# Performance work log

Hardware: AMD Instinct MI355X
Metric: run time of the kernel (lower is better)

The kernel has to match this reference:

```python
import jax, jax.numpy as jnp
import numpy as np

# ---- static configuration (mirrors EarthSpecificBlock/EarthAttention3D) ----
WS = (2, 6, 12)                 # window_size (Z, H, W)
DIM = 192
HEADS = 6
DEPTH = 2
B, Z, H, W = 1, 8, 91, 180      # token grid entering the layer
PAD_H = (WS[1] - H % WS[1]) % WS[1]   # 5
PAD_W = (WS[2] - W % WS[2]) % WS[2]   # 0
HP, WP = H + PAD_H, W + PAD_W         # 96, 180
TOK = WS[0] * WS[1] * WS[2]           # 144 tokens per window
NZ, NH, NW = Z // WS[0], HP // WS[1], WP // WS[2]   # 4, 16, 15
TYPE_W = NZ * NH                      # 64 window types (Z x lat)
BIAS_ROWS = (2 * WS[2] - 1) * WS[1] * WS[1] * WS[0] * WS[0]  # 3312


def _construct_index():
    """Position index into the earth-specific bias table (EarthAttention3D._construct_index)."""
    zi = np.arange(WS[0]); zj = -np.arange(WS[0]) * WS[0]
    hi = np.arange(WS[1]); hj = -np.arange(WS[1]) * WS[1]
    w = np.arange(WS[2])
    c1 = np.stack(np.meshgrid(zi, hi, w, indexing='ij')).reshape(3, -1)
    c2 = np.stack(np.meshgrid(zj, hj, w, indexing='ij')).reshape(3, -1)
    coords = (c1[:, :, None] - c2[:, None, :]).transpose(1, 2, 0)
    coords[:, :, 2] += WS[2] - 1
    coords[:, :, 1] *= 2 * WS[2] - 1
    coords[:, :, 0] *= (2 * WS[2] - 1) * WS[1] * WS[1]
    return coords.sum(-1).reshape(-1)   # (TOK*TOK,)


def _gen_mask():
    """Shifted-window attention mask (gen_mask), shape (1, NW, TYPE_W, 1, TOK, TOK)."""
    m = np.zeros((1, Z, HP, WP, 1), np.float32)
    zs = (slice(0, -WS[0]), slice(-WS[0], -WS[0] // 2), slice(-WS[0] // 2, None))
    hs = (slice(0, -WS[1]), slice(-WS[1], -WS[1] // 2), slice(-WS[1] // 2, None))
    cnt = 0
    for zsl in zs:
        for hsl in hs:
            m[:, zsl, hsl, :, :] = cnt
            cnt += 1
    mw = m.reshape(1, NZ, WS[0], NH, WS[1], NW, WS[2], 1).transpose(0, 1, 3, 5, 2, 4, 6, 7)
    mw = mw.reshape(1, NZ, NH, NW, TOK)
    am = mw[:, :, :, :, None, :] - mw[:, :, :, :, :, None]
    am = np.where(am != 0, np.float32(-100.0), np.float32(0.0))
    return am.transpose(0, 3, 1, 2, 4, 5).reshape(1, NW, TYPE_W, 1, TOK, TOK)


POS_IDX = jnp.asarray(_construct_index())
MASK = jnp.asarray(_gen_mask())


def _ln(x, g, b):
    m = x.mean(-1, keepdims=True)
    v = ((x - m) ** 2).mean(-1, keepdims=True)
    return (x - m) * jax.lax.rsqrt(v + 1e-5) * g + b


def _block(x, qkv_w, qkv_b, proj_w, proj_b, bias_tab, g1, b1, g2, b2, w1, bm1, w2, bm2, roll):
    shortcut = x
    x = jnp.pad(x, ((0, 0), (0, 0), (0, PAD_H), (0, PAD_W), (0, 0)))
    if roll:
        x = jnp.roll(x, (-(WS[0] // 2), -(WS[1] // 2), -(WS[2] // 2)), axis=(1, 2, 3))
    # window partition: (B, NW, TYPE_W, TOK, C)
    xw = x.reshape(B, NZ, WS[0], NH, WS[1], NW, WS[2], DIM).transpose(0, 5, 1, 3, 2, 4, 6, 7)
    xw = xw.reshape(B, NW, TYPE_W, TOK, DIM)
    dh = DIM // HEADS
    qkv = (xw @ qkv_w + qkv_b).reshape(B, NW, TYPE_W, TOK, 3, HEADS, dh)
    qkv = qkv.transpose(4, 0, 1, 2, 5, 3, 6)   # (3, B, NW, TYPE_W, HEADS, TOK, dh)
    q, k, v = qkv[0], qkv[1], qkv[2]
    q = q * (dh ** -0.5)
    attn = jnp.einsum('bwphid,bwphjd->bwphij', q, k)
    bias = bias_tab[POS_IDX].reshape(TOK, TOK, TYPE_W, HEADS).transpose(2, 3, 0, 1)
    attn = attn + bias
    if roll:
        attn = attn + MASK
    attn = jax.nn.softmax(attn, axis=-1)
    out = jnp.einsum('bwphij,bwphjd->bwphid', attn, v)
    out = out.transpose(0, 1, 2, 4, 3, 5).reshape(B, NW, TYPE_W, TOK, DIM)
    out = out @ proj_w + proj_b
    # window merge back to (B, Z, HP, WP, C)
    x = out.reshape(B, NW, NZ, NH, WS[0], WS[1], WS[2], DIM).transpose(0, 2, 4, 3, 5, 1, 6, 7)
    x = x.reshape(B, Z, HP, WP, DIM)
    if roll:
        x = jnp.roll(x, (WS[0] // 2, WS[1] // 2, WS[2] // 2), axis=(1, 2, 3))
    x = x[:, :, :H, :W]
    x = shortcut + _ln(x, g1, b1)           # post-norm residual, as in source
    h = jax.nn.gelu(x @ w1 + bm1, approximate=False)
    h = h @ w2 + bm2
    return x + _ln(h, g2, b2)


def setup_inputs() -> dict:
    key = jax.random.key(0)
    ks = jax.random.split(key, 8)
    s = 0.02
    return {
        'x': jax.random.normal(ks[0], (B, Z, H, W, DIM), jnp.float32),
        'qkv_w': jax.random.normal(ks[1], (DEPTH, DIM, 3 * DIM), jnp.float32) * s,
        'qkv_b': jnp.zeros((DEPTH, 3 * DIM), jnp.float32),
        'proj_w': jax.random.normal(ks[2], (DEPTH, DIM, DIM), jnp.float32) * s,
        'proj_b': jnp.zeros((DEPTH, DIM), jnp.float32),
        'bias_tab': jax.random.normal(ks[3], (DEPTH, BIAS_ROWS, TYPE_W, HEADS), jnp.float32) * s,
        'norm1_g': jnp.ones((DEPTH, DIM), jnp.float32),
        'norm1_b': jnp.zeros((DEPTH, DIM), jnp.float32),
        'norm2_g': jnp.ones((DEPTH, DIM), jnp.float32),
        'norm2_b': jnp.zeros((DEPTH, DIM), jnp.float32),
        'mlp_w1': jax.random.normal(ks[4], (DEPTH, DIM, 4 * DIM), jnp.float32) * s,
        'mlp_b1': jnp.zeros((DEPTH, 4 * DIM), jnp.float32),
        'mlp_w2': jax.random.normal(ks[5], (DEPTH, 4 * DIM, DIM), jnp.float32) * s,
        'mlp_b2': jnp.zeros((DEPTH, DIM), jnp.float32),
    }


def reference(x, qkv_w, qkv_b, proj_w, proj_b, bias_tab, norm1_g, norm1_b,
              norm2_g, norm2_b, mlp_w1, mlp_b1, mlp_w2, mlp_b2):
    for i in range(DEPTH):
        x = _block(x, qkv_w[i], qkv_b[i], proj_w[i], proj_b[i], bias_tab[i],
                   norm1_g[i], norm1_b[i], norm2_g[i], norm2_b[i],
                   mlp_w1[i], mlp_b1[i], mlp_w2[i], mlp_b2[i], roll=(i % 2 == 1))
    return x
```

## Files before the change

### kernel.cpp

```cpp
#include <hip/hip_runtime.h>
#include <math.h>

#define NTOK   131040
#define NTOKW  138240

typedef __attribute__((ext_vector_type(8))) short bf16x8;
typedef __attribute__((ext_vector_type(8))) unsigned short u16x8;
typedef __attribute__((ext_vector_type(4))) float f32x4;
typedef __attribute__((ext_vector_type(2))) float f32x2;

__device__ __forceinline__ float b2f(unsigned short u){
  union { unsigned u; float f; } v; v.u = ((unsigned)u) << 16; return v.f;
}
__device__ __forceinline__ unsigned short f2b(float f){
  union { float f; unsigned u; } v; v.f = f;
  unsigned r = v.u + 0x7FFFu + ((v.u >> 16) & 1u);
  return (unsigned short)(r >> 16);
}
__device__ __forceinline__ float gelu_fast(float x){
  float t = 0.79788456080286536f * (x + 0.044715f * x * x * x);
  float e = __expf(2.0f * t);
  float th = 1.0f - 2.0f * __builtin_amdgcn_rcpf(e + 1.0f);
  return 0.5f * x * (1.0f + th);
}
__device__ __forceinline__ unsigned pk_bf16(float lo, float hi){
  unsigned r;
  asm("v_cvt_pk_bf16_f32 %0, %1, %2" : "=v"(r) : "v"(lo), "v"(hi));
  return r;
}
__device__ __forceinline__ void lds_barrier(){
  asm volatile("s_waitcnt lgkmcnt(0)" ::: "memory");
  __builtin_amdgcn_sched_barrier(0);
  __builtin_amdgcn_s_barrier();
  __builtin_amdgcn_sched_barrier(0);
}

__global__ __launch_bounds__(256) void transp(const float* __restrict__ src,
                                              unsigned short* __restrict__ dst,
                                              int K, int N){
  int i = blockIdx.x*256 + threadIdx.x;
  if (i < K*N){
    int n = i / K, k = i % K;
    dst[i] = f2b(src[(size_t)k*N + n]);
  }
}

__global__ __launch_bounds__(256) void bias_pre(
    const float* __restrict__ btab,
    unsigned short* __restrict__ bw,
    int roll)
{
  int gid = blockIdx.x*256 + threadIdx.x;
  int e    = gid % 40;
  int rem  = gid / 40;
  int lane = rem % 64;
  int rem2 = rem / 64;
  int wv   = rem2 % 9;
  int slice= rem2 / 9;
  unsigned short out = 0;
  if (e < 36){
    int ct = e >> 2, r = e & 3;
    int i = wv*16 + (lane>>4)*4 + r;
    int j = ct*16 + (lane & 15);
    int tw = slice / 6, head = slice % 6;
    int ia = i/72, ib = (i%72)/12, ic = i%12;
    int ja = j/72, jb = (j%72)/12, jc = j%12;
    int idx = (ia + 2*ja)*828 + (ib + 6*jb)*23 + (ic - jc + 11);
    float v = btab[(size_t)idx*384 + tw*6 + head];
    if (roll){
      int nz = tw >> 4, nh = tw & 15;
      int zi = nz*2+ia, hi = nh*6+ib, zj = nz*2+ja, hj = nh*6+jb;
      int ri = 3*((zi<6)?0:((zi<7)?1:2)) + ((hi<90)?0:((hi<93)?1:2));
      int rj = 3*((zj<6)?0:((zj<7)?1:2)) + ((hj<90)?0:((hj<93)?1:2));
      if (ri != rj) v -= 100.0f;
    }
    out = f2b(v);
  }
  int vec = e >> 3, elem = e & 7;
  size_t di = ((((size_t)slice*9 + wv)*5 + vec)*64 + lane)*8 + elem;
  bw[di] = out;
}

__global__ __launch_bounds__(256) void gather_win(const float* __restrict__ x,
                                                  unsigned short* __restrict__ xw,
                                                  int roll){
  int gid = blockIdx.x*256 + threadIdx.x;
  int row = gid / 24;
  int dp  = gid % 24;
  int tok = row % 144;
  int wt  = row / 144;
  int tw  = wt & 63;
  int w   = wt >> 6;
  int nz = tw >> 4, nh = tw & 15;
  int wz = tok / 72; int rem = tok % 72; int wh = rem / 12; int ww = rem % 12;
  int z = nz*2 + wz, h = nh*6 + wh, wc = w*12 + ww;
  if (roll){ z = (z+1)&7; h = (h+3)%96; wc = (wc+6)%180; }
  int d0 = dp*8;
  u16x8 o;
  if (h < 91){
    const float* s = x + ((size_t)((z*91 + h)*180 + wc))*192 + d0;
    #pragma unroll
    for (int i=0;i<8;i++) o[i] = f2b(s[i]);
  } else {
    #pragma unroll
    for (int i=0;i<8;i++) o[i] = 0;
  }
  *(u16x8*)(xw + (size_t)row*192 + d0) = o;
}

__global__ __launch_bounds__(512) void gemm_k192(
    const unsigned short* __restrict__ A,
    const unsigned short* __restrict__ Bt,
    const float* __restrict__ bias,
    unsigned short* __restrict__ C,
    int N)
{
  __shared__ unsigned short Bst[192][200];
  int m0 = blockIdx.x * 128;
  int n0 = blockIdx.y * 192;
  int t = threadIdx.x;
  int lane = t & 63, w = t >> 6;
  int wm = w >> 2, wn = w & 3;
  int lg = lane >> 4, lr = lane & 15;

  #pragma unroll
  for (int i=0;i<9;i++){
    int idx = t + i*512;
    int r = idx / 24, c = (idx % 24)*8;
    *(u16x8*)&Bst[r][c] = *(const u16x8*)(Bt + (size_t)(n0 + r)*192 + c);
  }
  __syncthreads();

  const unsigned short* aRow = A + (size_t)(m0 + wm*64 + lr)*192 + lg*8;

  f32x4 acc[4][3];
  #pragma unroll
  for (int a=0;a<4;a++)
    #pragma unroll
    for (int b=0;b<3;b++) acc[a][b] = (f32x4){0.f,0.f,0.f,0.f};

  bf16x8 aP[2][6];
  #pragma unroll
  for (int ks=0; ks<6; ks++) aP[0][ks] = *(const bf16x8*)(aRow + ks*32);

  #pragma unroll
  for (int rt=0; rt<4; rt++){
    if (rt < 3){
      const unsigned short* an = aRow + (size_t)(rt+1)*16*192;
      #pragma unroll
      for (int ks=0; ks<6; ks++) aP[(rt+1)&1][ks] = *(const bf16x8*)(an + ks*32);
    }
    #pragma unroll
    for (int ks=0; ks<6; ks++){
      bf16x8 b0 = *(const bf16x8*)&Bst[wn*48 +      lr][ks*32 + lg*8];
      bf16x8 b1 = *(const bf16x8*)&Bst[wn*48 + 16 + lr][ks*32 + lg*8];
      bf16x8 b2 = *(const bf16x8*)&Bst[wn*48 + 32 + lr][ks*32 + lg*8];
      bf16x8 af = aP[rt&1][ks];
      acc[rt][0] = __builtin_amdgcn_mfma_f32_16x16x32_bf16(af, b0, acc[rt][0], 0,0,0);
      acc[rt][1] = __builtin_amdgcn_mfma_f32_16x16x32_bf16(af, b1, acc[rt][1], 0,0,0);
      acc[rt][2] = __builtin_amdgcn_mfma_f32_16x16x32_bf16(af, b2, acc[rt][2], 0,0,0);
    }
  }

  #pragma unroll
  for (int rt=0; rt<4; rt++){
    #pragma unroll
    for (int fn=0; fn<3; fn++){
      int colg = n0 + wn*48 + fn*16 + lr;
      float bv = bias[colg];
      #pragma unroll
      for (int r=0;r<4;r++){
        int rowg = m0 + wm*64 + rt*16 + lg*4 + r;
        C[(size_t)rowg*N + colg] = f2b(acc[rt][fn][r] + bv);
      }
    }
  }
}

__global__ __launch_bounds__(576) void attn_win(
    const unsigned short* __restrict__ qkv,
    const unsigned short* __restrict__ bw,
    unsigned short* __restrict__ outp)
{
  __shared__ union {
    struct { unsigned short Qs[144][32]; unsigned short Ks[144][40]; } qk;
    unsigned short Ps[144][160];
  } U;
  __shared__ unsigned short Vst[32][160];

  int b = blockIdx.x;
  int head = b % 6;
  int wt = b / 6;
  int tw = wt & 63;
  int t = threadIdx.x;
  int lane = t & 63;
  int wv = t >> 6;
  int lg = lane >> 4, lr = lane & 15;

  {
    int tok = t >> 2, c0 = (t & 3)*8;
    size_t base = ((size_t)wt*144 + tok)*576 + head*32 + c0;
    u16x8 qv = *(const u16x8*)(qkv + base);
    u16x8 kv = *(const u16x8*)(qkv + base + 192);
    u16x8 vv = *(const u16x8*)(qkv + base + 384);
    u16x8 qs;
    #pragma unroll
    for (int i=0;i<8;i++) qs[i] = f2b(b2f(qv[i]) * 0.17677669529663687f);
    *(u16x8*)&U.qk.Qs[tok][c0] = qs;
    *(u16x8*)&U.qk.Ks[tok][c0] = kv;
    #pragma unroll
    for (int i=0;i<8;i++) Vst[c0+i][tok] = vv[i];
  }
  if (t < 512) Vst[t >> 4][144 + (t & 15)] = 0;

  u16x8 bv0, bv1, bv2, bv3, bv4;
  {
    size_t sbase = ((((size_t)(tw*6 + head))*9 + wv)*5*64 + lane)*8;
    bv0 = *(const u16x8*)(bw + sbase);
    bv1 = *(const u16x8*)(bw + sbase + 64*8);
    bv2 = *(const u16x8*)(bw + sbase + 2*64*8);
    bv3 = *(const u16x8*)(bw + sbase + 3*64*8);
    bv4 = *(const u16x8*)(bw + sbase + 4*64*8);
  }
  __syncthreads();

  float s[9][4];
  {
    bf16x8 a = *(const bf16x8*)&U.qk.Qs[wv*16 + lr][lg*8];
    #pragma unroll
    for (int ct=0; ct<9; ct++){
      bf16x8 bb = *(const bf16x8*)&U.qk.Ks[ct*16 + lr][lg*8];
      f32x4 d = {0.f,0.f,0.f,0.f};
      d = __builtin_amdgcn_mfma_f32_16x16x32_bf16(a, bb, d, 0,0,0);
      s[ct][0]=d[0]; s[ct][1]=d[1]; s[ct][2]=d[2]; s[ct][3]=d[3];
    }
  }

  #pragma unroll
  for (int ct=0; ct<9; ct++){
    #pragma unroll
    for (int r=0;r<4;r++){
      const int e = ct*4 + r;
      unsigned short bu =
        (e < 8)  ? bv0[e & 7] :
        (e < 16) ? bv1[e & 7] :
        (e < 24) ? bv2[e & 7] :
        (e < 32) ? bv3[e & 7] : bv4[e & 7];
      s[ct][r] += b2f(bu);
    }
  }

  float mx[4] = {-1e30f,-1e30f,-1e30f,-1e30f};
  #pragma unroll
  for (int ct=0; ct<9; ct++)
    #pragma unroll
    for (int r=0;r<4;r++) mx[r] = fmaxf(mx[r], s[ct][r]);
  #pragma unroll
  for (int off=1; off<16; off<<=1)
    #pragma unroll
    for (int r=0;r<4;r++) mx[r] = fmaxf(mx[r], __shfl_xor(mx[r], off));
  float sm[4] = {0.f,0.f,0.f,0.f};
  #pragma unroll
  for (int ct=0; ct<9; ct++)
    #pragma unroll
    for (int r=0;r<4;r++){ s[ct][r] = __expf(s[ct][r] - mx[r]); sm[r] += s[ct][r]; }
  #pragma unroll
  for (int off=1; off<16; off<<=1)
    #pragma unroll
    for (int r=0;r<4;r++) sm[r] += __shfl_xor(sm[r], off);
  float inv[4];
  #pragma unroll
  for (int r=0;r<4;r++) inv[r] = 1.0f / sm[r];

  lds_barrier();

  #pragma unroll
  for (int ct=0; ct<9; ct++)
    #pragma unroll
    for (int r=0;r<4;r++)
      U.Ps[wv*16 + lg*4 + r][ct*16 + lr] = f2b(s[ct][r] * inv[r]);
  #pragma unroll
  for (int r=0;r<4;r++) U.Ps[wv*16 + lg*4 + r][144 + lr] = 0;
  __syncthreads();

  #pragma unroll
  for (int ct2=0; ct2<2; ct2++){
    f32x4 o = {0.f,0.f,0.f,0.f};
    #pragma unroll
    for (int kt=0; kt<5; kt++){
      bf16x8 a  = *(const bf16x8*)&U.Ps[wv*16 + lr][kt*32 + lg*8];
      bf16x8 bb = *(const bf16x8*)&Vst[ct2*16 + lr][kt*32 + lg*8];
      o = __builtin_amdgcn_mfma_f32_16x16x32_bf16(a, bb, o, 0,0,0);
    }
    size_t rb = ((size_t)wt*144 + wv*16 + lg*4)*192 + head*32 + ct2*16 + lr;
    #pragma unroll
    for (int r=0;r<4;r++) outp[rb + (size_t)r*192] = f2b(o[r]);
  }
}

__global__ __launch_bounds__(256) void unwin_ln(
  const unsigned short* __restrict__ ywin,
  const float* __restrict__ xsrc,
  const float* __restrict__ g, const float* __restrict__ bb,
  float* __restrict__ outf, unsigned short* __restrict__ outb, int roll)
{
  int tok = blockIdx.x*4 + (threadIdx.x>>6);
  if (tok >= NTOK) return;
  int lane = threadIdx.x & 63;
  int z = tok / (91*180);
  int rem = tok % (91*180);
  int h = rem / 180, wc = rem % 180;
  int zz=z, hh=h, ww=wc;
  if (roll){ zz = (z+7)&7; hh = (h+93)%96; ww = (wc+174)%180; }
  int nz = zz>>1, wz = zz&1;
  int nh = hh/6,  wh = hh%6;
  int nw = ww/12, w2 = ww%12;
  size_t row = ((size_t)(nw*64 + nz*16 + nh))*144 + wz*72 + wh*12 + w2;
  const unsigned short* yr = ywin + row*192;
  float v[3]; float s=0.f, ss=0.f;
  #pragma unroll
  for (int i=0;i<3;i++){ v[i] = b2f(yr[lane + i*64]); s += v[i]; ss += v[i]*v[i]; }
  #pragma unroll
  for (int off=32; off>=1; off>>=1){ s += __shfl_xor(s, off); ss += __shfl_xor(ss, off); }
  float mean = s * (1.0f/192.0f);
  float var = ss * (1.0f/192.0f) - mean*mean;
  float rinv = rsqrtf(var + 1e-5f);
  size_t tb = (size_t)tok*192;
  #pragma unroll
  for (int i=0;i<3;i++){
    int d = lane + i*64;
    float o = xsrc[tb + d] + ((v[i]-mean)*rinv*g[d] + bb[d]);
    outf[tb+d] = o;
    outb[tb+d] = f2b(o);
  }
}

__global__ __launch_bounds__(256) void mlp_fused_ln(
    const unsigned short* __restrict__ A,
    const unsigned short* __restrict__ W1t,
    const float* __restrict__ bias1,
    const unsigned short* __restrict__ W2t,
    const float* __restrict__ mbias2,
    const float* __restrict__ xmid,
    const float* __restrict__ lng,
    const float* __restrict__ lnb,
    float* __restrict__ outF,
    int M)
{
  __shared__ unsigned short W1s[32][204];
  __shared__ unsigned short W2s[192][44];
  __shared__ unsigned short Hs[4][32][40];
  __shared__ float b1s[768];
  __shared__ float eps[576];
  int m0 = blockIdx.x*128;
  int t = threadIdx.x, lane = t & 63, w = t >> 6;
  int lg = lane >> 4, lr = lane & 15;

  bf16x8 afrA[6], afrB[6];
  {
    int ra = m0 + w*32 + lr, rb = ra + 16;
    if (ra < M){
      const unsigned short* ap = A + (size_t)ra*192 + lg*8;
      #pragma unroll
      for (int ks=0; ks<6; ks++) afrA[ks] = *(const bf16x8*)(ap + ks*32);
    } else {
      #pragma unroll
      for (int ks=0; ks<6; ks++)
        #pragma unroll
        for (int j=0;j<8;j++) afrA[ks][j] = 0;
    }
    if (rb < M){
      const unsigned short* ap = A + (size_t)rb*192 + lg*8;
      #pragma unroll
      for (int ks=0; ks<6; ks++) afrB[ks] = *(const bf16x8*)(ap + ks*32);
    } else {
      #pragma unroll
      for (int ks=0; ks<6; ks++)
        #pragma unroll
        for (int j=0;j<8;j++) afrB[ks][j] = 0;
    }
  }

  b1s[t] = bias1[t];
  b1s[t + 256] = bias1[t + 256];
  b1s[t + 512] = bias1[t + 512];
  if (t < 192){ eps[t] = mbias2[t]; eps[192 + t] = lng[t]; eps[384 + t] = lnb[t]; }

  int i1r[3], i1c[3], i2r[3], i2c[3];
  #pragma unroll
  for (int i=0;i<3;i++){
    int idx = t + i*256;
    i1r[i] = idx/24; i1c[i] = (idx%24)*8;
    i2r[i] = idx/4;  i2c[i] = (idx&3)*8;
  }

  u16x8 w1r[3], w2r[3];
  #pragma unroll
  for (int i=0;i<3;i++){
    w1r[i] = *(const u16x8*)(W1t + (size_t)i1r[i]*192 + i1c[i]);
    w2r[i] = *(const u16x8*)(W2t + (size_t)i2r[i]*768 + i2c[i]);
  }

  f32x4 accA[12], accB[12];
  #pragma unroll
  for (int i=0;i<12;i++){ accA[i] = (f32x4){0.f,0.f,0.f,0.f}; accB[i] = (f32x4){0.f,0.f,0.f,0.f}; }

  for (int it=0; it<24; ++it){
    int hc = it*32;
    #pragma unroll
    for (int i=0;i<3;i++){
      *(u16x8*)&W1s[i1r[i]][i1c[i]] = w1r[i];
      *(u16x8*)&W2s[i2r[i]][i2c[i]] = w2r[i];
    }
    if (it < 23){
      int hc2 = hc + 32;
      #pragma unroll
      for (int i=0;i<3;i++){
        w1r[i] = *(const u16x8*)(W1t + (size_t)(hc2 + i1r[i])*192 + i1c[i]);
        w2r[i] = *(const u16x8*)(W2t + (size_t)i2r[i]*768 + hc2 + i2c[i]);
      }
    }
    lds_barrier();

    f32x4 h0a = (f32x4){0.f,0.f,0.f,0.f}, h1a = h0a, h0b = h0a, h1b = h0a;
    #pragma unroll
    for (int ks=0; ks<6; ks++){
      bf16x8 b0  = *(const bf16x8*)&W1s[2*lr    ][ks*32 + lg*8];
      bf16x8 b1f = *(const bf16x8*)&W1s[2*lr + 1][ks*32 + lg*8];
      h0a = __builtin_amdgcn_mfma_f32_16x16x32_bf16(afrA[ks], b0,  h0a, 0,0,0);
      h1a = __builtin_amdgcn_mfma_f32_16x16x32_bf16(afrA[ks], b1f, h1a, 0,0,0);
      h0b = __builtin_amdgcn_mfma_f32_16x16x32_bf16(afrB[ks], b0,  h0b, 0,0,0);
      h1b = __builtin_amdgcn_mfma_f32_16x16x32_bf16(afrB[ks], b1f, h1b, 0,0,0);
    }
    float bb0 = b1s[hc + 2*lr];
    float bb1 = b1s[hc + 2*lr + 1];
    #pragma unroll
    for (int r=0;r<4;r++){
      *(unsigned*)&Hs[w][lg*4 + r][2*lr] =
          pk_bf16(gelu_fast(h0a[r] + bb0), gelu_fast(h1a[r] + bb1));
      *(unsigned*)&Hs[w][16 + lg*4 + r][2*lr] =
          pk_bf16(gelu_fast(h0b[r] + bb0), gelu_fast(h1b[r] + bb1));
    }
    bf16x8 paA = *(const bf16x8*)&Hs[w][lr][lg*8];
    bf16x8 paB = *(const bf16x8*)&Hs[w][16 + lr][lg*8];
    #pragma unroll
    for (int f=0; f<6; f++){
      bf16x8 c0 = *(const bf16x8*)&W2s[f*32 + 2*lr    ][lg*8];
      bf16x8 c1 = *(const bf16x8*)&W2s[f*32 + 2*lr + 1][lg*8];
      accA[2*f]   = __builtin_amdgcn_mfma_f32_16x16x32_bf16(paA, c0, accA[2*f],   0,0,0);
      accA[2*f+1] = __builtin_amdgcn_mfma_f32_16x16x32_bf16(paA, c1, accA[2*f+1], 0,0,0);
      accB[2*f]   = __builtin_amdgcn_mfma_f32_16x16x32_bf16(paB, c0, accB[2*f],   0,0,0);
      accB[2*f+1] = __builtin_amdgcn_mfma_f32_16x16x32_bf16(paB, c1, accB[2*f+1], 0,0,0);
    }
    lds_barrier();
  }

  #pragma unroll
  for (int gsel=0; gsel<2; gsel++){
    f32x4* acc = gsel ? accB : accA;
    #pragma unroll
    for (int r=0;r<4;r++){
      int row = m0 + w*32 + gsel*16 + lg*4 + r;
      float s = 0.f, ss = 0.f;
      #pragma unroll
      for (int f=0; f<6; f++){
        float v0 = acc[2*f][r]   + eps[f*32 + 2*lr];
        float v1 = acc[2*f+1][r] + eps[f*32 + 2*lr + 1];
        s += v0 + v1; ss += v0*v0 + v1*v1;
      }
      #pragma unroll
      for (int off=1; off<16; off<<=1){ s += __shfl_xor(s, off); ss += __shfl_xor(ss, off); }
      float mean = s * (1.0f/192.0f);
      float var  = ss * (1.0f/192.0f) - mean*mean;
      float rinv = rsqrtf(var + 1e-5f);
      if (row < M){
        size_t base = (size_t)row*192;
        #pragma unroll
        for (int f=0; f<6; f++){
          int c0 = f*32 + 2*lr;
          float v0 = acc[2*f][r]   + eps[c0];
          float v1 = acc[2*f+1][r] + eps[c0 + 1];
          f32x2 xm = *(const f32x2*)&xmid[base + c0];
          f32x2 o;
          o[0] = xm[0] + (v0 - mean)*rinv*eps[192 + c0]     + eps[384 + c0];
          o[1] = xm[1] + (v1 - mean)*rinv*eps[192 + c0 + 1] + eps[384 + c0 + 1];
          *(f32x2*)&outF[base + c0] = o;
        }
      }
    }
  }
}

extern "C" void kernel_launch(void* const* d_in, const int* in_sizes, int n_in,
                              void* d_out, int out_size, void* d_ws, size_t ws_size,
                              hipStream_t stream)
{
  const float* x_in    = (const float*)d_in[0];
  const float* qkvw    = (const float*)d_in[1];
  const float* qkvbias = (const float*)d_in[2];
  const float* projw   = (const float*)d_in[3];
  const float* projbias= (const float*)d_in[4];
  const float* btab    = (const float*)d_in[5];
  const float* n1g = (const float*)d_in[6];
  const float* n1b = (const float*)d_in[7];
  const float* n2g = (const float*)d_in[8];
  const float* n2b = (const float*)d_in[9];
  const float* w1  = (const float*)d_in[10];
  const float* b1  = (const float*)d_in[11];
  const float* w2  = (const float*)d_in[12];
  const float* b2  = (const float*)d_in[13];
  float* outp = (float*)d_out;

  const size_t REG_A = (size_t)NTOKW*192;
  const size_t REG_B = (size_t)NTOKW*576;
  const size_t W_QT  = (size_t)2*576*192;
  const size_t W_PT  = (size_t)2*192*192;
  const size_t W_1T  = (size_t)2*768*192;
  const size_t W_2T  = (size_t)2*192*768;
  const size_t TOT_SH = REG_A + REG_B + W_QT + W_PT + W_1T + W_2T;
  const size_t NEEDED = TOT_SH*2 + (size_t)NTOK*192*4;
  if (ws_size < NEEDED) return;

  unsigned short* ws16 = (unsigned short*)d_ws;
  size_t off = 0;
  unsigned short* regA = ws16 + off; off += REG_A;
  unsigned short* regB = ws16 + off; off += REG_B;
  unsigned short* wqt  = ws16 + off; off += W_QT;
  unsigned short* wpt  = ws16 + off; off += W_PT;
  unsigned short* w1t  = ws16 + off; off += W_1T;
  unsigned short* w2t  = ws16 + off; off += W_2T;
  float* xmidf = (float*)(ws16 + off);
  unsigned short* bw = (unsigned short*)xmidf;

  for (int dep=0; dep<2; dep++){
    transp<<<(192*576+255)/256,256,0,stream>>>(qkvw + (size_t)dep*192*576,
                                               wqt + (size_t)dep*576*192, 192, 576);
    transp<<<(192*192+255)/256,256,0,stream>>>(projw + (size_t)dep*192*192,
                                               wpt + (size_t)dep*192*192, 192, 192);
    transp<<<(192*768+255)/256,256,0,stream>>>(w1 + (size_t)dep*192*768,
                                               w1t + (size_t)dep*768*192, 192, 768);
    transp<<<(768*192+255)/256,256,0,stream>>>(w2 + (size_t)dep*768*192,
                                               w2t + (size_t)dep*192*768, 768, 192);
  }

  for (int dep=0; dep<2; dep++){
    int roll = dep;
    const float* xs = (dep==0) ? x_in : outp;
    float* xout = outp;

    gather_win<<<NTOKW*24/256, 256, 0, stream>>>(xs, regA, roll);

    dim3 g1(NTOKW/128, 3);
    gemm_k192<<<g1, 512, 0, stream>>>(regA, wqt + (size_t)dep*576*192,
                                      qkvbias + dep*576, regB, 576);

    bias_pre<<<(384*9*64*40)/256, 256, 0, stream>>>(btab + (size_t)dep*3312*384, bw, roll);

    attn_win<<<960*6, 576, 0, stream>>>(regB, bw, regA);

    dim3 g2(NTOKW/128, 1);
    gemm_k192<<<g2, 512, 0, stream>>>(regA, wpt + (size_t)dep*192*192,
                                      projbias + dep*192, regB, 192);

    unwin_ln<<<NTOK/4, 256, 0, stream>>>(regB, xs, n1g + dep*192, n1b + dep*192,
                                         xmidf, regA, roll);

    mlp_fused_ln<<<(NTOK+127)/128, 256, 0, stream>>>(
        regA, w1t + (size_t)dep*768*192, b1 + dep*768,
        w2t + (size_t)dep*192*768, b2 + dep*192,
        xmidf, n2g + dep*192, n2b + dep*192, xout, NTOK);
  }
}
```

Before: 1.185 ms.

## Double-buffer MLP weight tiles and software-pipeline first GEMM ahead of second

```diff
diff --git a/kernel.cpp b/kernel.cpp
--- a/kernel.cpp
+++ b/kernel.cpp
@@ -335,7 +335,7 @@
   }
 }
 
-__global__ __launch_bounds__(256) void mlp_fused_ln(
+__global__ __launch_bounds__(512) void mlp_fused_ln(
     const unsigned short* __restrict__ A,
     const unsigned short* __restrict__ W1t,
     const float* __restrict__ bias1,
@@ -347,12 +347,12 @@
     float* __restrict__ outF,
     int M)
 {
-  __shared__ unsigned short W1s[32][204];
-  __shared__ unsigned short W2s[192][44];
-  __shared__ unsigned short Hs[4][32][40];
+  __shared__ unsigned short W1s[2][32][196];
+  __shared__ unsigned short W2s[2][192][44];
+  __shared__ unsigned short Hs[8][32][40];
   __shared__ float b1s[768];
   __shared__ float eps[576];
-  int m0 = blockIdx.x*128;
+  int m0 = blockIdx.x*256;
   int t = threadIdx.x, lane = t & 63, w = t >> 6;
   int lg = lane >> 4, lr = lane & 15;
 
@@ -382,56 +382,75 @@
   }
 
   b1s[t] = bias1[t];
-  b1s[t + 256] = bias1[t + 256];
-  b1s[t + 512] = bias1[t + 512];
+  if (t < 256) b1s[512 + t] = bias1[512 + t];
   if (t < 192){ eps[t] = mbias2[t]; eps[192 + t] = lng[t]; eps[384 + t] = lnb[t]; }
 
-  int i1r[3], i1c[3], i2r[3], i2c[3];
-  #pragma unroll
-  for (int i=0;i<3;i++){
-    int idx = t + i*256;
+  int i1r[2], i1c[2], i2r[2], i2c[2];
+  #pragma unroll
+  for (int i=0;i<2;i++){
+    int idx = t + i*512;
     i1r[i] = idx/24; i1c[i] = (idx%24)*8;
     i2r[i] = idx/4;  i2c[i] = (idx&3)*8;
   }
-
-  u16x8 w1r[3], w2r[3];
-  #pragma unroll
-  for (int i=0;i<3;i++){
-    w1r[i] = *(const u16x8*)(W1t + (size_t)i1r[i]*192 + i1c[i]);
-    w2r[i] = *(const u16x8*)(W2t + (size_t)i2r[i]*768 + i2c[i]);
-  }
+  bool g2nd = (t + 512) < 768;
+
+  {
+    *(u16x8*)&W1s[0][i1r[0]][i1c[0]] = *(const u16x8*)(W1t + (size_t)i1r[0]*192 + i1c[0]);
+    *(u16x8*)&W1s[1][i1r[0]][i1c[0]] = *(const u16x8*)(W1t + (size_t)(32 + i1r[0])*192 + i1c[0]);
+    *(u16x8*)&W2s[0][i2r[0]][i2c[0]] = *(const u16x8*)(W2t + (size_t)i2r[0]*768 + i2c[0]);
+    if (g2nd){
+      *(u16x8*)&W1s[0][i1r[1]][i1c[1]] = *(const u16x8*)(W1t + (size_t)i1r[1]*192 + i1c[1]);
+      *(u16x8*)&W1s[1][i1r[1]][i1c[1]] = *(const u16x8*)(W1t + (size_t)(32 + i1r[1])*192 + i1c[1]);
+      *(u16x8*)&W2s[0][i2r[1]][i2c[1]] = *(const u16x8*)(W2t + (size_t)i2r[1]*768 + i2c[1]);
+    }
+  }
+  lds_barrier();
+
+  u16x8 w1r[2], w2r[2];
+  w1r[0] = *(const u16x8*)(W1t + (size_t)(64 + i1r[0])*192 + i1c[0]);
+  w2r[0] = *(const u16x8*)(W2t + (size_t)i2r[0]*768 + 32 + i2c[0]);
+  if (g2nd){
+    w1r[1] = *(const u16x8*)(W1t + (size_t)(64 + i1r[1])*192 + i1c[1]);
+    w2r[1] = *(const u16x8*)(W2t + (size_t)i2r[1]*768 + 32 + i2c[1]);
+  }
+
+  f32x4 h0a = (f32x4){0.f,0.f,0.f,0.f}, h1a = h0a, h0b = h0a, h1b = h0a;
+  #pragma unroll
+  for (int ks=0; ks<6; ks++){
+    bf16x8 b0  = *(const bf16x8*)&W1s[0][2*lr    ][ks*32 + lg*8];
+    bf16x8 b1f = *(const bf16x8*)&W1s[0][2*lr + 1][ks*32 + lg*8];
+    h0a = __builtin_amdgcn_mfma_f32_16x16x32_bf16(afrA[ks], b0,  h0a, 0,0,0);
+    h1a = __builtin_amdgcn_mfma_f32_16x16x32_bf16(afrA[ks], b1f, h1a, 0,0,0);
+    h0b = __builtin_amdgcn_mfma_f32_16x16x32_bf16(afrB[ks], b0,  h0b, 0,0,0);
+    h1b = __builtin_amdgcn_mfma_f32_16x16x32_bf16(afrB[ks], b1f, h1b, 0,0,0);
+  }
+  lds_barrier();
 
   f32x4 accA[12], accB[12];
   #pragma unroll
   for (int i=0;i<12;i++){ accA[i] = (f32x4){0.f,0.f,0.f,0.f}; accB[i] = (f32x4){0.f,0.f,0.f,0.f}; }
 
   for (int it=0; it<24; ++it){
+    int cur = it & 1, nxt = cur ^ 1;
+
+    if (it < 22){
+      *(u16x8*)&W1s[cur][i1r[0]][i1c[0]] = w1r[0];
+      if (g2nd) *(u16x8*)&W1s[cur][i1r[1]][i1c[1]] = w1r[1];
+    }
+    if (it < 23){
+      *(u16x8*)&W2s[nxt][i2r[0]][i2c[0]] = w2r[0];
+      if (g2nd) *(u16x8*)&W2s[nxt][i2r[1]][i2c[1]] = w2r[1];
+    }
+    if (it < 21){
+      w1r[0] = *(const u16x8*)(W1t + (size_t)((it+3)*32 + i1r[0])*192 + i1c[0]);
+      if (g2nd) w1r[1] = *(const u16x8*)(W1t + (size_t)((it+3)*32 + i1r[1])*192 + i1c[1]);
+    }
+    if (it < 22){
+      w2r[0] = *(const u16x8*)(W2t + (size_t)i2r[0]*768 + (it+2)*32 + i2c[0]);
+      if (g2nd) w2r[1] = *(const u16x8*)(W2t + (size_t)i2r[1]*768 + (it+2)*32 + i2c[1]);
+    }
+
     int hc = it*32;
-    #pragma unroll
-    for (int i=0;i<3;i++){
-      *(u16x8*)&W1s[i1r[i]][i1c[i]] = w1r[i];
-      *(u16x8*)&W2s[i2r[i]][i2c[i]] = w2r[i];
-    }
-    if (it < 23){
-      int hc2 = hc + 32;
-      #pragma unroll
-      for (int i=0;i<3;i++){
-        w1r[i] = *(const u16x8*)(W1t + (size_t)(hc2 + i1r[i])*192 + i1c[i]);
-        w2r[i] = *(const u16x8*)(W2t + (size_t)i2r[i]*768 + hc2 + i2c[i]);
-      }
-    }
-    lds_barrier();
-
-    f32x4 h0a = (f32x4){0.f,0.f,0.f,0.f}, h1a = h0a, h0b = h0a, h1b = h0a;
-    #pragma unroll
-    for (int ks=0; ks<6; ks++){
-      bf16x8 b0  = *(const bf16x8*)&W1s[2*lr    ][ks*32 + lg*8];
-      bf16x8 b1f = *(const bf16x8*)&W1s[2*lr + 1][ks*32 + lg*8];
-      h0a = __builtin_amdgcn_mfma_f32_16x16x32_bf16(afrA[ks], b0,  h0a, 0,0,0);
-      h1a = __builtin_amdgcn_mfma_f32_16x16x32_bf16(afrA[ks], b1f, h1a, 0,0,0);
-      h0b = __builtin_amdgcn_mfma_f32_16x16x32_bf16(afrB[ks], b0,  h0b, 0,0,0);
-      h1b = __builtin_amdgcn_mfma_f32_16x16x32_bf16(afrB[ks], b1f, h1b, 0,0,0);
-    }
     float bb0 = b1s[hc + 2*lr];
     float bb1 = b1s[hc + 2*lr + 1];
     #pragma unroll
@@ -443,15 +462,31 @@
     }
     bf16x8 paA = *(const bf16x8*)&Hs[w][lr][lg*8];
     bf16x8 paB = *(const bf16x8*)&Hs[w][16 + lr][lg*8];
+
+    f32x4 hn0a = (f32x4){0.f,0.f,0.f,0.f}, hn1a = hn0a, hn0b = hn0a, hn1b = hn0a;
+    if (it < 23){
+      #pragma unroll
+      for (int ks=0; ks<6; ks++){
+        bf16x8 b0  = *(const bf16x8*)&W1s[nxt][2*lr    ][ks*32 + lg*8];
+        bf16x8 b1f = *(const bf16x8*)&W1s[nxt][2*lr + 1][ks*32 + lg*8];
+        hn0a = __builtin_amdgcn_mfma_f32_16x16x32_bf16(afrA[ks], b0,  hn0a, 0,0,0);
+        hn1a = __builtin_amdgcn_mfma_f32_16x16x32_bf16(afrA[ks], b1f, hn1a, 0,0,0);
+        hn0b = __builtin_amdgcn_mfma_f32_16x16x32_bf16(afrB[ks], b0,  hn0b, 0,0,0);
+        hn1b = __builtin_amdgcn_mfma_f32_16x16x32_bf16(afrB[ks], b1f, hn1b, 0,0,0);
+      }
+    }
+
     #pragma unroll
     for (int f=0; f<6; f++){
-      bf16x8 c0 = *(const bf16x8*)&W2s[f*32 + 2*lr    ][lg*8];
-      bf16x8 c1 = *(const bf16x8*)&W2s[f*32 + 2*lr + 1][lg*8];
+      bf16x8 c0 = *(const bf16x8*)&W2s[cur][f*32 + 2*lr    ][lg*8];
+      bf16x8 c1 = *(const bf16x8*)&W2s[cur][f*32 + 2*lr + 1][lg*8];
       accA[2*f]   = __builtin_amdgcn_mfma_f32_16x16x32_bf16(paA, c0, accA[2*f],   0,0,0);
       accA[2*f+1] = __builtin_amdgcn_mfma_f32_16x16x32_bf16(paA, c1, accA[2*f+1], 0,0,0);
       accB[2*f]   = __builtin_amdgcn_mfma_f32_16x16x32_bf16(paB, c0, accB[2*f],   0,0,0);
       accB[2*f+1] = __builtin_amdgcn_mfma_f32_16x16x32_bf16(paB, c1, accB[2*f+1], 0,0,0);
     }
+
+    h0a = hn0a; h1a = hn1a; h0b = hn0b; h1b = hn1b;
     lds_barrier();
   }
 
@@ -565,7 +600,7 @@
     unwin_ln<<<NTOK/4, 256, 0, stream>>>(regB, xs, n1g + dep*192, n1b + dep*192,
                                          xmidf, regA, roll);
 
-    mlp_fused_ln<<<(NTOK+127)/128, 256, 0, stream>>>(
+    mlp_fused_ln<<<(NTOK+255)/256, 512, 0, stream>>>(
         regA, w1t + (size_t)dep*768*192, b1 + dep*768,
         w2t + (size_t)dep*192*768, b2 + dep*192,
         xmidf, n2g + dep*192, n2b + dep*192, xout, NTOK);
```

Result: faster. 1.053 ms (-11.2%).
